# Kernel tuning notes

Hardware: AMD Instinct MI355X
Metric: run time of the kernel (lower is better)

Reference implementation:

```python
import jax, jax.numpy as jnp
import numpy as np

N = 100_000      # nodes
E = 1_600_000    # edges (avg degree 16)
IN = 128         # in_features
F = 64           # out_features
H = 1            # num_heads (module's broadcasting only valid for H==1)
S = 1            # num_samples
SLOPE = 0.2      # leaky relu negative slope


def setup_inputs() -> dict:
    key = jax.random.key(0)
    ks = jax.random.split(key, 6)
    feat = jax.random.normal(ks[0], (N, IN), jnp.float32)
    src = jax.random.randint(ks[1], (E,), 0, N)
    dst = jax.random.randint(ks[2], (E,), 0, N)
    noise = jax.random.normal(ks[3], (E, S, H, 1), jnp.float32)  # rsample noise
    W_fc = jax.random.normal(ks[4], (IN, H * F), jnp.float32) / np.sqrt(IN)
    W_post = jax.random.normal(ks[5], (F, 4), jnp.float32) / np.sqrt(F)
    b_post = jnp.zeros((4,), jnp.float32)
    bias = jnp.zeros((H, F), jnp.float32)
    return dict(feat=feat, W_fc=W_fc, W_post=W_post, b_post=b_post,
                bias=bias, noise=noise, src=src, dst=dst)


def reference(feat, W_fc, W_post, b_post, bias, noise, src, dst):
    # node projection: [N, IN] -> [N, H, F]
    h = (feat @ W_fc).reshape(N, H, F)
    # posterior params: [N, H, 4] -> four [N, H, 1]
    pp = h @ W_post + b_post
    loc_l, loc_r, lsl, lsr = jnp.split(pp, 4, axis=-1)
    # per-edge u_add_v gathers
    loc_e = loc_l[src] + loc_r[dst]                       # [E, H, 1]
    loc_e = jnp.where(loc_e >= 0, loc_e, SLOPE * loc_e)   # leaky relu
    scale_e = jnp.exp(lsl[src] + lsr[dst])                # [E, H, 1]
    # reparameterized sample: [E, S, H, 1]
    e = loc_e[:, None] + scale_e[:, None] * noise
    # edge softmax over incoming edges of each dst node
    emax = jax.ops.segment_max(e, dst, num_segments=N)
    e_exp = jnp.exp(e - emax[dst])
    esum = jax.ops.segment_sum(e_exp, dst, num_segments=N)
    a = e_exp / esum[dst]                                 # [E, S, H, 1]
    a = jnp.swapaxes(a, 1, -1)                            # [E, 1, H, S]
    # u_mul_e then scatter-sum to dst: [E, H, F, 1] * [E, 1, H, S]
    m = h[src][..., None] * a                             # [E, H, F, S] (H==1)
    rst = jax.ops.segment_sum(m, dst, num_segments=N)     # [N, H, F, S]
    return rst + bias[..., None]
```

## Files before the change

kernel.cpp:

```cpp
#include <hip/hip_runtime.h>
#include <math.h>

#define NSLOPE 0.2f
#define ASTRIDE 136
#define CSH 10
#define NCB 128
#define EPB 2048
#define K4T 512
#define EPT 4
#define FSPLIT 16
#define SCH 1152

typedef __attribute__((ext_vector_type(8))) short bf16x8;
typedef __attribute__((ext_vector_type(4))) short bf16x4;
typedef __attribute__((ext_vector_type(4))) float f32x4;

__device__ __forceinline__ unsigned short f2bf(float x) {
    unsigned u = __float_as_uint(x);
    u += 0x7fffu + ((u >> 16) & 1u);
    return (unsigned short)(u >> 16);
}

__global__ __launch_bounds__(128) void kW(const float* __restrict__ wfc,
                                          const float* __restrict__ wpost,
                                          float4* __restrict__ wc) {
    __shared__ float wp_s[256];
    int t = threadIdx.x;
    wp_s[t] = wpost[t];
    wp_s[128 + t] = wpost[128 + t];
    __syncthreads();
    float a0 = 0.f, a1 = 0.f, a2 = 0.f, a3 = 0.f;
    for (int n = 0; n < 64; n++) {
        float w = wfc[t * 64 + n];
        a0 += w * wp_s[n * 4 + 0]; a1 += w * wp_s[n * 4 + 1];
        a2 += w * wp_s[n * 4 + 2]; a3 += w * wp_s[n * 4 + 3];
    }
    float4 o; o.x = a0; o.y = a1; o.z = a2; o.w = a3;
    wc[t] = o;
}

__global__ __launch_bounds__(256) void k1_mfma(
    const float* __restrict__ feat, const float* __restrict__ wfc,
    float4* __restrict__ h_g, int n)
{
    __shared__ unsigned short a_s[64 * ASTRIDE];
    __shared__ unsigned short b_s[64 * ASTRIDE];
    int t = threadIdx.x;
    int row0 = blockIdx.x * 64;
    for (int i = t; i < 2048; i += 256) {
        int row = i >> 5, c4 = (i & 31) * 4;
        float4 f = {0.f, 0.f, 0.f, 0.f};
        if (row0 + row < n) f = ((const float4*)(feat + (long)(row0 + row) * 128))[i & 31];
        bf16x4 b4;
        b4.x = (short)f2bf(f.x); b4.y = (short)f2bf(f.y);
        b4.z = (short)f2bf(f.z); b4.w = (short)f2bf(f.w);
        *(bf16x4*)(a_s + row * ASTRIDE + c4) = b4;
    }
    for (int i = t; i < 2048; i += 256) {
        int k = i >> 4, n0 = (i & 15) * 4;
        float4 f = ((const float4*)wfc)[i];
        b_s[(n0 + 0) * ASTRIDE + k] = f2bf(f.x);
        b_s[(n0 + 1) * ASTRIDE + k] = f2bf(f.y);
        b_s[(n0 + 2) * ASTRIDE + k] = f2bf(f.z);
        b_s[(n0 + 3) * ASTRIDE + k] = f2bf(f.w);
    }
    __syncthreads();
    int lane = t & 63, wv = t >> 6;
    int c = lane & 15, quad = lane >> 4;
    f32x4 acc[4] = {{0.f,0.f,0.f,0.f},{0.f,0.f,0.f,0.f},{0.f,0.f,0.f,0.f},{0.f,0.f,0.f,0.f}};
    int arow = wv * 16 + c;
    #pragma unroll
    for (int kb = 0; kb < 4; kb++) {
        int ko = kb * 32 + quad * 8;
        bf16x8 af = *(const bf16x8*)(a_s + arow * ASTRIDE + ko);
        #pragma unroll
        for (int tt = 0; tt < 4; tt++) {
            bf16x8 bf = *(const bf16x8*)(b_s + (tt * 16 + c) * ASTRIDE + ko);
            acc[tt] = __builtin_amdgcn_mfma_f32_16x16x32_bf16(af, bf, acc[tt], 0, 0, 0);
        }
    }
    __syncthreads();
    unsigned short* h_s = a_s;
    #pragma unroll
    for (int tt = 0; tt < 4; tt++)
        #pragma unroll
        for (int r = 0; r < 4; r++)
            h_s[(wv * 16 + quad * 4 + r) * 64 + tt * 16 + c] = f2bf(acc[tt][r]);
    __syncthreads();
    for (int i = t; i < 512; i += 256) {
        int row = i >> 3;
        if (row0 + row < n)
            h_g[(long)(row0 + row) * 8 + (i & 7)] = *(const float4*)(h_s + row * 64 + (i & 7) * 8);
    }
}

__global__ __launch_bounds__(256) void k1b_pp(
    const float* __restrict__ feat, const float4* __restrict__ wc,
    const float* __restrict__ bpost, float4* __restrict__ pp,
    int* __restrict__ gcnt, int* __restrict__ fcnt, int NC, int N)
{
    int gid = blockIdx.x * 256 + threadIdx.x;
    if (gid < NC) gcnt[gid] = 0;
    if (gid < NC * 16) fcnt[gid] = 0;
    int wid = gid >> 6;
    int lane = threadIdx.x & 63;
    if (wid >= N) return;
    const float* fr = feat + (long)wid * 128;
    float f0 = fr[lane], f1 = fr[64 + lane];
    float4 w0 = wc[lane], w1 = wc[64 + lane];
    float p0 = f0 * w0.x + f1 * w1.x;
    float p1 = f0 * w0.y + f1 * w1.y;
    float p2 = f0 * w0.z + f1 * w1.z;
    float p3 = f0 * w0.w + f1 * w1.w;
    #pragma unroll
    for (int off = 1; off < 64; off <<= 1) {
        p0 += __shfl_xor(p0, off);
        p1 += __shfl_xor(p1, off);
        p2 += __shfl_xor(p2, off);
        p3 += __shfl_xor(p3, off);
    }
    if (lane == 0) {
        float4 bp = *((const float4*)bpost);
        float4 o;
        o.x = p0 + bp.x; o.y = p1 + bp.y; o.z = p2 + bp.z; o.w = p3 + bp.w;
        pp[wid] = o;
    }
}

__global__ __launch_bounds__(K4T) void k4a(
    const int* __restrict__ src, const int* __restrict__ dst,
    const float* __restrict__ noise, const float4* __restrict__ pp,
    int* __restrict__ gcnt, float2* __restrict__ cbuf, int E, int NC, int CCAP)
{
    __shared__ float    s_ev[EPB];
    __shared__ unsigned s_key[EPB];
    __shared__ unsigned char s_bin[EPB];
    __shared__ int hist[NCB], lbase[NCB], lcur[NCB], gdelta[NCB];
    __shared__ int wtot;
    int t = threadIdx.x;
    long e0 = (long)blockIdx.x * EPB;
    int d[EPT]; bool ok[EPT];
    for (int i = t; i < NCB; i += K4T) hist[i] = 0;
    __syncthreads();
    #pragma unroll
    for (int u = 0; u < EPT; u++) {
        long e = e0 + t + u * K4T;
        ok[u] = e < E;
        d[u] = ok[u] ? __builtin_nontemporal_load(dst + e) : 0;
        if (ok[u]) atomicAdd(&hist[d[u] >> CSH], 1);
    }
    __syncthreads();
    int v = (t < NCB) ? hist[t] : 0;
    int inc = v;
    #pragma unroll
    for (int off = 1; off < 64; off <<= 1) {
        int u2 = __shfl_up(inc, off);
        if ((t & 63) >= off) inc += u2;
    }
    if (t == 63) wtot = inc;
    __syncthreads();
    if (t < NCB) {
        int base = (t >= 64) ? wtot : 0;
        int lb = inc - v + base;
        lbase[t] = lb; lcur[t] = lb;
        if (t < NC && v > 0) {
            int gb = atomicAdd(&gcnt[t], v);
            gdelta[t] = gb - lb;
        }
    }
    __syncthreads();
    #pragma unroll
    for (int u = 0; u < EPT; u++) {
        if (!ok[u]) continue;
        long e = e0 + t + u * K4T;
        int s = __builtin_nontemporal_load(src + e);
        float nz = __builtin_nontemporal_load(noise + e);
        float4 ps = pp[s], pd = pp[d[u]];
        float loc = ps.x + pd.y;
        loc = loc >= 0.f ? loc : NSLOPE * loc;
        float ev = loc + __expf(ps.z + pd.w) * nz;
        int bin = d[u] >> CSH;
        int pos = atomicAdd(&lcur[bin], 1);
        s_ev[pos] = ev;
        s_key[pos] = (unsigned)s | ((unsigned)(d[u] & 1023) << 17);
        s_bin[pos] = (unsigned char)bin;
    }
    __syncthreads();
    long rem = (long)E - e0;
    int btot = rem < EPB ? (int)rem : EPB;
    for (int i = t; i < btot; i += K4T) {
        int bin = s_bin[i];
        int gpos = gdelta[bin] + i;
        if (gpos < CCAP) {
            float2 r; r.x = s_ev[i]; r.y = __uint_as_float(s_key[i]);
            cbuf[(long)bin * CCAP + gpos] = r;
        }
    }
}

__global__ __launch_bounds__(256) void k4b(
    const int* __restrict__ gcnt, const float2* __restrict__ cbuf,
    int* __restrict__ fcnt, float2* __restrict__ fbuf, int CCAP, int FCAP)
{
    __shared__ float    s_ev[SCH], s_ev2[SCH];
    __shared__ unsigned s_key[SCH], s_sr2[SCH];
    __shared__ unsigned char s_sub[SCH], s_sub2[SCH];
    __shared__ int h16[16], b16[16], cur16[16], gd16[16];
    int t = threadIdx.x;
    int c = blockIdx.x >> 4, j = blockIdx.x & 15;
    int cnt = gcnt[c]; if (cnt > CCAP) cnt = CCAP;
    int chunk = (cnt + FSPLIT - 1) / FSPLIT;
    int i0 = j * chunk;
    int i1 = i0 + chunk; if (i1 > cnt) i1 = cnt;
    int n = i1 - i0; if (n < 0) n = 0;
    if (t < 16) { h16[t] = 0; cur16[t] = 0; }
    __syncthreads();
    for (int i = t; i < n; i += 256) {
        float2 r = cbuf[(long)c * CCAP + i0 + i];
        unsigned key = __float_as_uint(r.y);
        int sub = (key >> 23) & 15;
        s_ev[i] = r.x; s_key[i] = key; s_sub[i] = (unsigned char)sub;
        atomicAdd(&h16[sub], 1);
    }
    __syncthreads();
    if (t == 0) {
        int run = 0;
        #pragma unroll
        for (int p = 0; p < 16; p++) { b16[p] = run; run += h16[p]; }
    }
    __syncthreads();
    if (t < 16 && h16[t] > 0)
        gd16[t] = atomicAdd(&fcnt[c * 16 + t], h16[t]) - b16[t];
    __syncthreads();
    for (int i = t; i < n; i += 256) {
        int sub = s_sub[i];
        int pos = b16[sub] + atomicAdd(&cur16[sub], 1);
        unsigned key = s_key[i];
        unsigned s  = key & 0x1FFFFu;
        unsigned dl = (key >> 17) & 63u;
        s_ev2[pos] = s_ev[i];
        s_sr2[pos] = s | (dl << 26);
        s_sub2[pos] = (unsigned char)sub;
    }
    __syncthreads();
    for (int i = t; i < n; i += 256) {
        int sub = s_sub2[i];
        int gpos = gd16[sub] + i;
        if (gpos < FCAP) {
            float2 r; r.x = s_ev2[i]; r.y = __uint_as_float(s_sr2[i]);
            fbuf[(long)(c * 16 + sub) * FCAP + gpos] = r;
        }
    }
}

__global__ __launch_bounds__(256) void k56_node(
    const int* __restrict__ fcnt, const float2* __restrict__ fbuf,
    const uint4* __restrict__ h8, const float* __restrict__ bias,
    float4* __restrict__ out4, int FCAP, int N)
{
    __shared__ float    o_ev[1344 + 8];
    __shared__ unsigned o_sr[1344 + 8];
    __shared__ int c[64], ox[64], c2[64];
    int t = threadIdx.x;
    int b = blockIdx.x;
    int n0 = b << 6;
    int cnt = fcnt[b]; if (cnt > FCAP) cnt = FCAP;
    const float2* rp = fbuf + (long)b * FCAP;
    if (t < 64) { c[t] = 0; c2[t] = 0; }
    __syncthreads();
    for (int i = t; i < cnt; i += 256)
        atomicAdd(&c[__float_as_uint(rp[i].y) >> 26], 1);
    __syncthreads();
    if (t < 64) {
        int val = c[t], inc = val;
        #pragma unroll
        for (int off = 1; off < 64; off <<= 1) {
            int u = __shfl_up(inc, off);
            if (t >= off) inc += u;
        }
        ox[t] = inc - val;
    }
    __syncthreads();
    for (int i = t; i < cnt; i += 256) {
        float2 v = rp[i];
        unsigned pk = __float_as_uint(v.y);
        int dl = pk >> 26;
        int pos = ox[dl] + atomicAdd(&c2[dl], 1);
        o_ev[pos] = v.x;
        o_sr[pos] = pk & 0x03FFFFFFu;
    }
    __syncthreads();
    {
        int nn4 = t >> 2, q = t & 3;
        int cn = c[nn4];
        int i0 = ox[nn4];
        float m = -INFINITY;
        for (int i = q; i < cn; i += 4) m = fmaxf(m, o_ev[i0 + i]);
        m = fmaxf(m, __shfl_xor(m, 1));
        m = fmaxf(m, __shfl_xor(m, 2));
        float ss = 0.f;
        for (int i = q; i < cn; i += 4) {
            float w = __expf(o_ev[i0 + i] - m);
            o_ev[i0 + i] = w;
            ss += w;
        }
        ss += __shfl_xor(ss, 1);
        ss += __shfl_xor(ss, 2);
        float inv = 1.f / ss;
        for (int i = q; i < cn; i += 4) o_ev[i0 + i] *= inv;
    }
    __syncthreads();
    int lane = t & 63, wv = t >> 6;
    int ch = lane & 7, sub = lane >> 3;
    for (int r = 0; r < 16; r += 2) {
        int nnA = wv * 16 + r, nnB = nnA + 1;
        int nodeA = n0 + nnA, nodeB = n0 + nnB;
        int cA = (nodeA < N) ? c[nnA] : 0;
        int cB = (nodeB < N) ? c[nnB] : 0;
        int iA = ox[nnA], iB = ox[nnB];
        float a0[8] = {0.f,0.f,0.f,0.f,0.f,0.f,0.f,0.f};
        float a1[8] = {0.f,0.f,0.f,0.f,0.f,0.f,0.f,0.f};
        int mx = cA > cB ? cA : cB;
        for (int jb = 0; jb < mx; jb += 16) {
            bool vA0 = (jb + sub) < cA, vA1 = (jb + 8 + sub) < cA;
            bool vB0 = (jb + sub) < cB, vB1 = (jb + 8 + sub) < cB;
            int jA0 = vA0 ? iA + jb + sub     : 0;
            int jA1 = vA1 ? iA + jb + 8 + sub : 0;
            int jB0 = vB0 ? iB + jb + sub     : 0;
            int jB1 = vB1 ? iB + jb + 8 + sub : 0;
            float wA0 = vA0 ? o_ev[jA0] : 0.f; int sA0 = vA0 ? (int)o_sr[jA0] : 0;
            float wA1 = vA1 ? o_ev[jA1] : 0.f; int sA1 = vA1 ? (int)o_sr[jA1] : 0;
            float wB0 = vB0 ? o_ev[jB0] : 0.f; int sB0 = vB0 ? (int)o_sr[jB0] : 0;
            float wB1 = vB1 ? o_ev[jB1] : 0.f; int sB1 = vB1 ? (int)o_sr[jB1] : 0;
            uint4 pA0 = h8[(long)sA0 * 8 + ch];
            uint4 pA1 = h8[(long)sA1 * 8 + ch];
            uint4 pB0 = h8[(long)sB0 * 8 + ch];
            uint4 pB1 = h8[(long)sB1 * 8 + ch];
            a0[0] += wA0 * __uint_as_float(pA0.x << 16);
            a0[1] += wA0 * __uint_as_float(pA0.x & 0xffff0000u);
            a0[2] += wA0 * __uint_as_float(pA0.y << 16);
            a0[3] += wA0 * __uint_as_float(pA0.y & 0xffff0000u);
            a0[4] += wA0 * __uint_as_float(pA0.z << 16);
            a0[5] += wA0 * __uint_as_float(pA0.z & 0xffff0000u);
            a0[6] += wA0 * __uint_as_float(pA0.w << 16);
            a0[7] += wA0 * __uint_as_float(pA0.w & 0xffff0000u);
            a0[0] += wA1 * __uint_as_float(pA1.x << 16);
            a0[1] += wA1 * __uint_as_float(pA1.x & 0xffff0000u);
            a0[2] += wA1 * __uint_as_float(pA1.y << 16);
            a0[3] += wA1 * __uint_as_float(pA1.y & 0xffff0000u);
            a0[4] += wA1 * __uint_as_float(pA1.z << 16);
            a0[5] += wA1 * __uint_as_float(pA1.z & 0xffff0000u);
            a0[6] += wA1 * __uint_as_float(pA1.w << 16);
            a0[7] += wA1 * __uint_as_float(pA1.w & 0xffff0000u);
            a1[0] += wB0 * __uint_as_float(pB0.x << 16);
            a1[1] += wB0 * __uint_as_float(pB0.x & 0xffff0000u);
            a1[2] += wB0 * __uint_as_float(pB0.y << 16);
            a1[3] += wB0 * __uint_as_float(pB0.y & 0xffff0000u);
            a1[4] += wB0 * __uint_as_float(pB0.z << 16);
            a1[5] += wB0 * __uint_as_float(pB0.z & 0xffff0000u);
            a1[6] += wB0 * __uint_as_float(pB0.w << 16);
            a1[7] += wB0 * __uint_as_float(pB0.w & 0xffff0000u);
            a1[0] += wB1 * __uint_as_float(pB1.x << 16);
            a1[1] += wB1 * __uint_as_float(pB1.x & 0xffff0000u);
            a1[2] += wB1 * __uint_as_float(pB1.y << 16);
            a1[3] += wB1 * __uint_as_float(pB1.y & 0xffff0000u);
            a1[4] += wB1 * __uint_as_float(pB1.z << 16);
            a1[5] += wB1 * __uint_as_float(pB1.z & 0xffff0000u);
            a1[6] += wB1 * __uint_as_float(pB1.w << 16);
            a1[7] += wB1 * __uint_as_float(pB1.w & 0xffff0000u);
        }
        #pragma unroll
        for (int off = 8; off < 64; off <<= 1)
            #pragma unroll
            for (int i = 0; i < 8; i++) {
                a0[i] += __shfl_xor(a0[i], off);
                a1[i] += __shfl_xor(a1[i], off);
            }
        if (sub == 0) {
            const float* bl = bias + ch * 8;
            if (nodeA < N) {
                f32x4 o0, o1;
                o0[0] = a0[0] + bl[0]; o0[1] = a0[1] + bl[1]; o0[2] = a0[2] + bl[2]; o0[3] = a0[3] + bl[3];
                o1[0] = a0[4] + bl[4]; o1[1] = a0[5] + bl[5]; o1[2] = a0[6] + bl[6]; o1[3] = a0[7] + bl[7];
                __builtin_nontemporal_store(o0, (f32x4*)(out4 + (long)nodeA * 16 + ch * 2));
                __builtin_nontemporal_store(o1, (f32x4*)(out4 + (long)nodeA * 16 + ch * 2 + 1));
            }
            if (nodeB < N) {
                f32x4 o0, o1;
                o0[0] = a1[0] + bl[0]; o0[1] = a1[1] + bl[1]; o0[2] = a1[2] + bl[2]; o0[3] = a1[3] + bl[3];
                o1[0] = a1[4] + bl[4]; o1[1] = a1[5] + bl[5]; o1[2] = a1[6] + bl[6]; o1[3] = a1[7] + bl[7];
                __builtin_nontemporal_store(o0, (f32x4*)(out4 + (long)nodeB * 16 + ch * 2));
                __builtin_nontemporal_store(o1, (f32x4*)(out4 + (long)nodeB * 16 + ch * 2 + 1));
            }
        }
    }
}

extern "C" void kernel_launch(void* const* d_in, const int* in_sizes, int n_in,
                              void* d_out, int out_size, void* d_ws, size_t ws_size,
                              hipStream_t stream) {
    const float* feat  = (const float*)d_in[0];
    const float* wfc   = (const float*)d_in[1];
    const float* wpost = (const float*)d_in[2];
    const float* bpost = (const float*)d_in[3];
    const float* bias  = (const float*)d_in[4];
    const float* noise = (const float*)d_in[5];
    const int*   src   = (const int*)d_in[6];
    const int*   dst   = (const int*)d_in[7];
    int N = in_sizes[0] / 128;
    int E = in_sizes[6];
    int NC = (N + 1023) >> 10;
    int NB = (N + 63) >> 6;
    int ECB = (E + NC - 1) / NC;
    int CCAP = (ECB + 8 * (int)sqrtf((float)ECB) + 71) & ~7;
    int EB  = (int)((long)E * 64 / N);
    int FCAP = (EB + 8 * (int)sqrtf((float)EB) + 39) & ~7;
    if (FCAP > 1344) FCAP = 1344;

    float*  ws   = (float*)d_ws;
    float2* cbuf = (float2*)ws;
    float2* fbuf = (float2*)(ws + (size_t)2 * NC * CCAP);
    float*  h    = ws + (size_t)2 * NC * CCAP + (size_t)2 * NB * FCAP;
    float4* pp   = (float4*)(h + (size_t)32 * N);
    int*    gcnt = (int*)(h + (size_t)32 * N + (size_t)4 * N);
    int*    fcnt = gcnt + 256;
    float4* wc   = (float4*)(fcnt + 2048);

    hipLaunchKernelGGL(kW, dim3(1), dim3(128), 0, stream, wfc, wpost, wc);
    hipLaunchKernelGGL(k1_mfma, dim3((N + 63) / 64), dim3(256), 0, stream,
                       feat, wfc, (float4*)h, N);
    hipLaunchKernelGGL(k1b_pp, dim3((N + 3) / 4), dim3(256), 0, stream,
                       feat, wc, bpost, pp, gcnt, fcnt, NC, N);
    hipLaunchKernelGGL(k4a, dim3((E + EPB - 1) / EPB), dim3(K4T), 0, stream,
                       src, dst, noise, pp, gcnt, cbuf, E, NC, CCAP);
    hipLaunchKernelGGL(k4b, dim3(NC * FSPLIT), dim3(256), 0, stream,
                       gcnt, cbuf, fcnt, fbuf, CCAP, FCAP);
    hipLaunchKernelGGL(k56_node, dim3(NB), dim3(256), 0, stream,
                       fcnt, fbuf, (const uint4*)h, bias, (float4*)d_out, FCAP, N);
}
```

Baseline: 256.1 us.

## Replace global atomic bucket counters with per-block fixed-capacity slots and prefix scan

The edge binning kernel no longer reserves space in each coarse bucket with a global atomicAdd. Each block now writes its per-bin count to a counts table and its edges to a fixed slot region of CAPB entries per (bin, block). The second-stage kernel prefix-scans the counts of its block range and locates each element's source slot with a binary search. This removes global atomic contention and the gcnt zeroing, at the cost of a sparser intermediate buffer, a per-element binary search, and silent loss of edges if any block puts more than CAPB edges into one bin.

```diff
diff --git a/kernel.cpp b/kernel.cpp
--- a/kernel.cpp
+++ b/kernel.cpp
@@ -8,6 +8,8 @@
 #define EPB 2048
 #define K4T 512
 #define EPT 4
+#define CAPB 48
+#define CBSTR 128
 #define FSPLIT 16
 #define SCH 1152
 
@@ -97,10 +99,9 @@
 __global__ __launch_bounds__(256) void k1b_pp(
     const float* __restrict__ feat, const float4* __restrict__ wc,
     const float* __restrict__ bpost, float4* __restrict__ pp,
-    int* __restrict__ gcnt, int* __restrict__ fcnt, int NC, int N)
+    int* __restrict__ fcnt, int NC, int N)
 {
     int gid = blockIdx.x * 256 + threadIdx.x;
-    if (gid < NC) gcnt[gid] = 0;
     if (gid < NC * 16) fcnt[gid] = 0;
     int wid = gid >> 6;
     int lane = threadIdx.x & 63;
@@ -130,15 +131,16 @@
 __global__ __launch_bounds__(K4T) void k4a(
     const int* __restrict__ src, const int* __restrict__ dst,
     const float* __restrict__ noise, const float4* __restrict__ pp,
-    int* __restrict__ gcnt, float2* __restrict__ cbuf, int E, int NC, int CCAP)
+    int* __restrict__ counts, float2* __restrict__ cbuf, int E, int NC, int NBLK)
 {
     __shared__ float    s_ev[EPB];
     __shared__ unsigned s_key[EPB];
     __shared__ unsigned char s_bin[EPB];
-    __shared__ int hist[NCB], lbase[NCB], lcur[NCB], gdelta[NCB];
+    __shared__ int hist[NCB], lbase[NCB], lcur[NCB];
     __shared__ int wtot;
     int t = threadIdx.x;
-    long e0 = (long)blockIdx.x * EPB;
+    int blk = blockIdx.x;
+    long e0 = (long)blk * EPB;
     int d[EPT]; bool ok[EPT];
     for (int i = t; i < NCB; i += K4T) hist[i] = 0;
     __syncthreads();
@@ -163,10 +165,7 @@
         int base = (t >= 64) ? wtot : 0;
         int lb = inc - v + base;
         lbase[t] = lb; lcur[t] = lb;
-        if (t < NC && v > 0) {
-            int gb = atomicAdd(&gcnt[t], v);
-            gdelta[t] = gb - lb;
-        }
+        if (t < NC) counts[blk * CBSTR + t] = v;
     }
     __syncthreads();
     #pragma unroll
@@ -190,33 +189,55 @@
     int btot = rem < EPB ? (int)rem : EPB;
     for (int i = t; i < btot; i += K4T) {
         int bin = s_bin[i];
-        int gpos = gdelta[bin] + i;
-        if (gpos < CCAP) {
+        int slot = i - lbase[bin];
+        if (slot < CAPB) {
             float2 r; r.x = s_ev[i]; r.y = __uint_as_float(s_key[i]);
-            cbuf[(long)bin * CCAP + gpos] = r;
+            cbuf[((long)bin * NBLK + blk) * CAPB + slot] = r;
         }
     }
 }
 
 __global__ __launch_bounds__(256) void k4b(
-    const int* __restrict__ gcnt, const float2* __restrict__ cbuf,
-    int* __restrict__ fcnt, float2* __restrict__ fbuf, int CCAP, int FCAP)
+    const int* __restrict__ counts, const float2* __restrict__ cbuf,
+    int* __restrict__ fcnt, float2* __restrict__ fbuf, int NC, int NBLK, int FCAP)
 {
     __shared__ float    s_ev[SCH], s_ev2[SCH];
     __shared__ unsigned s_key[SCH], s_sr2[SCH];
     __shared__ unsigned char s_sub[SCH], s_sub2[SCH];
     __shared__ int h16[16], b16[16], cur16[16], gd16[16];
+    __shared__ int pfx[65];
+    __shared__ int ntot;
     int t = threadIdx.x;
     int c = blockIdx.x >> 4, j = blockIdx.x & 15;
-    int cnt = gcnt[c]; if (cnt > CCAP) cnt = CCAP;
-    int chunk = (cnt + FSPLIT - 1) / FSPLIT;
-    int i0 = j * chunk;
-    int i1 = i0 + chunk; if (i1 > cnt) i1 = cnt;
-    int n = i1 - i0; if (n < 0) n = 0;
+    int per = (NBLK + FSPLIT - 1) / FSPLIT;
+    int blk0 = j * per;
+    int nb = NBLK - blk0; if (nb > per) nb = per; if (nb < 0) nb = 0;
     if (t < 16) { h16[t] = 0; cur16[t] = 0; }
-    __syncthreads();
+    if (t < 64) {
+        int cb = 0;
+        if (t < nb) {
+            cb = counts[(blk0 + t) * CBSTR + c];
+            if (cb > CAPB) cb = CAPB;
+        }
+        int inc = cb;
+        #pragma unroll
+        for (int off = 1; off < 64; off <<= 1) {
+            int u = __shfl_up(inc, off);
+            if (t >= off) inc += u;
+        }
+        pfx[t] = inc - cb;
+        if (t == 63) { pfx[64] = inc; ntot = inc; }
+    }
+    __syncthreads();
+    int n = ntot; if (n > SCH) n = SCH;
     for (int i = t; i < n; i += 256) {
-        float2 r = cbuf[(long)c * CCAP + i0 + i];
+        int lo = 0, hi = nb;
+        while (hi - lo > 1) {
+            int mid = (lo + hi) >> 1;
+            if (pfx[mid] <= i) lo = mid; else hi = mid;
+        }
+        int slot = i - pfx[lo];
+        float2 r = cbuf[((long)c * NBLK + blk0 + lo) * CAPB + slot];
         unsigned key = __float_as_uint(r.y);
         int sub = (key >> 23) & 15;
         s_ev[i] = r.x; s_key[i] = key; s_sub[i] = (unsigned char)sub;
@@ -411,30 +432,29 @@
     int E = in_sizes[6];
     int NC = (N + 1023) >> 10;
     int NB = (N + 63) >> 6;
-    int ECB = (E + NC - 1) / NC;
-    int CCAP = (ECB + 8 * (int)sqrtf((float)ECB) + 71) & ~7;
+    int NBLK = (E + EPB - 1) / EPB;
     int EB  = (int)((long)E * 64 / N);
     int FCAP = (EB + 8 * (int)sqrtf((float)EB) + 39) & ~7;
     if (FCAP > 1344) FCAP = 1344;
 
-    float*  ws   = (float*)d_ws;
-    float2* cbuf = (float2*)ws;
-    float2* fbuf = (float2*)(ws + (size_t)2 * NC * CCAP);
-    float*  h    = ws + (size_t)2 * NC * CCAP + (size_t)2 * NB * FCAP;
-    float4* pp   = (float4*)(h + (size_t)32 * N);
-    int*    gcnt = (int*)(h + (size_t)32 * N + (size_t)4 * N);
-    int*    fcnt = gcnt + 256;
-    float4* wc   = (float4*)(fcnt + 2048);
+    float*  ws     = (float*)d_ws;
+    float2* cbuf   = (float2*)ws;
+    float2* fbuf   = (float2*)(ws + (size_t)2 * NC * NBLK * CAPB);
+    float*  h      = ws + (size_t)2 * NC * NBLK * CAPB + (size_t)2 * NB * FCAP;
+    float4* pp     = (float4*)(h + (size_t)32 * N);
+    int*    counts = (int*)(h + (size_t)32 * N + (size_t)4 * N);
+    int*    fcnt   = counts + (size_t)NBLK * CBSTR;
+    float4* wc     = (float4*)(fcnt + 2048);
 
     hipLaunchKernelGGL(kW, dim3(1), dim3(128), 0, stream, wfc, wpost, wc);
     hipLaunchKernelGGL(k1_mfma, dim3((N + 63) / 64), dim3(256), 0, stream,
                        feat, wfc, (float4*)h, N);
     hipLaunchKernelGGL(k1b_pp, dim3((N + 3) / 4), dim3(256), 0, stream,
-                       feat, wc, bpost, pp, gcnt, fcnt, NC, N);
-    hipLaunchKernelGGL(k4a, dim3((E + EPB - 1) / EPB), dim3(K4T), 0, stream,
-                       src, dst, noise, pp, gcnt, cbuf, E, NC, CCAP);
+                       feat, wc, bpost, pp, fcnt, NC, N);
+    hipLaunchKernelGGL(k4a, dim3(NBLK), dim3(K4T), 0, stream,
+                       src, dst, noise, pp, counts, cbuf, E, NC, NBLK);
     hipLaunchKernelGGL(k4b, dim3(NC * FSPLIT), dim3(256), 0, stream,
-                       gcnt, cbuf, fcnt, fbuf, CCAP, FCAP);
+                       counts, cbuf, fcnt, fbuf, NC, NBLK, FCAP);
     hipLaunchKernelGGL(k56_node, dim3(NB), dim3(256), 0, stream,
                        fcnt, fbuf, (const uint4*)h, bias, (float4*)d_out, FCAP, N);
 }
```

Result: faster. 245.3 us (-4.2%).
